# Optimization experiments

Measured on AMD Instinct MI355X. Metric: run time of the kernel, lower is better.

## Reference

```python
import jax, jax.numpy as jnp
import numpy as np

OUT_F = 8192
IN_F = 8192
RANK = 32
N_TOK = 128


def _pack_ternary(w_q):
    """Pack int8 ternary {-1,0,+1} [out,in] -> uint8 [out,in//4], LSB-first 2-bit codes."""
    enc = (w_q.astype(np.int32) + 1).astype(np.uint8).reshape(w_q.shape[0], -1, 4)
    packed = enc[:, :, 0] | (enc[:, :, 1] << 2) | (enc[:, :, 2] << 4) | (enc[:, :, 3] << 6)
    return packed


def setup_inputs() -> dict:
    key = jax.random.key(0)
    kx, kw, ks, ka, kb, kbias = jax.random.split(key, 6)
    x = jax.random.normal(kx, (N_TOK, IN_F), dtype=jnp.float32)
    # ternary weights in {-1,0,+1}
    w_q = np.asarray(jax.random.randint(kw, (OUT_F, IN_F), -1, 2, dtype=jnp.int32), dtype=np.int8)
    weight_packed = jnp.asarray(_pack_ternary(w_q), dtype=jnp.uint8)
    scale = jax.random.uniform(ks, (OUT_F,), dtype=jnp.float32, minval=0.01, maxval=0.05)
    lora_A = jax.random.normal(ka, (OUT_F, RANK), dtype=jnp.float32) * 0.02
    lora_B = jax.random.normal(kb, (RANK, IN_F), dtype=jnp.float32) * 0.02
    bias = jax.random.normal(kbias, (OUT_F,), dtype=jnp.float32) * 0.01
    return {"x": x, "weight_packed": weight_packed, "scale": scale,
            "lora_A": lora_A, "lora_B": lora_B, "bias": bias, "in_features": IN_F}


def _unpack_ternary(packed, in_features, dtype):
    # packed: uint8 [out, in//4]; LSB-first 2-bit codes, code-1 -> {-1,0,+1}
    p = packed.astype(jnp.int32)
    vals = jnp.stack([p & 3, (p >> 2) & 3, (p >> 4) & 3, (p >> 6) & 3], axis=-1)
    vals = vals.reshape(packed.shape[0], -1)[:, :in_features] - 1
    return vals.astype(dtype)


def reference(x, weight_packed, scale, lora_A, lora_B, bias, in_features):
    W = _unpack_ternary(weight_packed, in_features, x.dtype)  # [out, in]
    out = (x @ W.T) * scale[None, :]                          # [n, out]
    out = out + (x @ lora_B.T) @ lora_A.T                     # low-rank LoRA path
    out = out + bias
    return out
```

## Files before the change

kernel.cpp:

```cpp
#include <hip/hip_runtime.h>
#include <hip/hip_bf16.h>
#include <stdint.h>

typedef float f32x4 __attribute__((ext_vector_type(4)));
typedef __bf16 bf16x8 __attribute__((ext_vector_type(8)));
typedef unsigned short ushort8 __attribute__((ext_vector_type(8)));

#define N_TOK 128
#define OUT_F 8192
#define IN_F  8192
#define RANK  32

#define KSPLIT 16
#define KB    (IN_F / KSPLIT)
#define BK    64
#define NSTEP (KB / BK)
#define WSTRIDE 16
#define LKC   4

#define XB_OFF 0
#define TB_OFF ((size_t)N_TOK * IN_F * 2)
#define PO_OFF (TB_OFF + (size_t)LKC * N_TOK * RANK * 4)

__device__ __forceinline__ unsigned short bf16r(float f) {
    uint32_t u = __float_as_uint(f);
    return (unsigned short)((u + 0x7FFFu + ((u >> 16) & 1u)) >> 16);
}

__global__ __launch_bounds__(256) void cvt_x(const float* __restrict__ x,
                                             unsigned short* __restrict__ xb) {
    size_t i = ((size_t)blockIdx.x * 256 + threadIdx.x) * 8;
    float4 a = *(const float4*)(x + i);
    float4 b = *(const float4*)(x + i + 4);
    ushort8 o;
    o[0] = bf16r(a.x); o[1] = bf16r(a.y); o[2] = bf16r(a.z); o[3] = bf16r(a.w);
    o[4] = bf16r(b.x); o[5] = bf16r(b.y); o[6] = bf16r(b.z); o[7] = bf16r(b.w);
    *(ushort8*)(xb + i) = o;
}

__global__ __launch_bounds__(256) void lora_t(const float* __restrict__ x,
                                              const float* __restrict__ lb,
                                              float* __restrict__ tB) {
    __shared__ float ts[256][33];
    __shared__ float ps[8][32];
    const int m = blockIdx.x >> 2, kc = blockIdx.x & 3;
    const int tid = threadIdx.x;
    const int c0 = kc * 2048 + tid * 8;
    float4 xv0 = *(const float4*)(x + (size_t)m * IN_F + c0);
    float4 xv1 = *(const float4*)(x + (size_t)m * IN_F + c0 + 4);
#pragma unroll
    for (int r = 0; r < RANK; ++r) {
        const float4* bp = (const float4*)(lb + (size_t)r * IN_F + c0);
        float4 b0 = bp[0], b1 = bp[1];
        float s = xv0.x * b0.x + xv0.y * b0.y + xv0.z * b0.z + xv0.w * b0.w +
                  xv1.x * b1.x + xv1.y * b1.y + xv1.z * b1.z + xv1.w * b1.w;
        ts[tid][r] = s;
    }
    __syncthreads();
    {
        int g = tid >> 5, r = tid & 31;
        float s = 0.f;
        for (int j = 0; j < 32; ++j) s += ts[g * 32 + j][r];
        ps[g][r] = s;
    }
    __syncthreads();
    if (tid < 32) {
        float s = 0.f;
#pragma unroll
        for (int g = 0; g < 8; ++g) s += ps[g][tid];
        tB[(kc * N_TOK + m) * RANK + tid] = s;
    }
}

__device__ __forceinline__ void decodeW(int4 v, uint32_t d[8]) {
    uint32_t p = (uint32_t)v.x | ((uint32_t)v.y << 8) |
                 ((uint32_t)v.z << 16) | ((uint32_t)v.w << 24);
    const uint32_t HI = 0x403F00BFu;
    const uint32_t LO = 0x00800080u;
#pragma unroll
    for (int j = 0; j < 8; ++j) {
        uint32_t c0 = (p >> (4 * j)) & 3u;
        uint32_t c1 = (p >> (4 * j + 2)) & 3u;
        uint32_t t = c0 | (c1 << 16);
        uint32_t sel = (t | (t << 8)) + 0x04000400u;
        d[j] = __builtin_amdgcn_perm(HI, LO, sel);
    }
}

__device__ __forceinline__ int swz(int row, int col) { return col ^ ((row & 7) << 3); }

__global__ __launch_bounds__(256) void ternary_gemm(const unsigned short* __restrict__ xb,
                                                    const int* __restrict__ wp,
                                                    unsigned short* __restrict__ pO) {
    __shared__ unsigned short xs[128][64];
    __shared__ unsigned short ww[128][64];
    const int tid = threadIdx.x;
    const int nb = blockIdx.x >> 4;
    const int ks = blockIdx.x & 15;
    const int n0 = nb * 128;
    const int k0 = ks * KB;
    const int lane = tid & 63;
    const int wid = tid >> 6;
    const int wr = wid >> 1, wc = wid & 1;

    const int srow = tid >> 2;
    const int xcol = (tid & 3) * 16;
    const unsigned short* xg0 = xb + (size_t)srow * IN_F + k0 + xcol;
    const unsigned short* xg1 = xg0 + (size_t)64 * IN_F;
    const int pcol = (tid & 3) * 4;
    const int* pg0 = wp + (size_t)(n0 + srow) * (IN_F / 4) + (k0 >> 2) + pcol;
    const int* pg1 = pg0 + (size_t)64 * (IN_F / 4);

    f32x4 acc[4][4];
#pragma unroll
    for (int i = 0; i < 4; ++i)
#pragma unroll
        for (int j = 0; j < 4; ++j) acc[i][j] = (f32x4){0.f, 0.f, 0.f, 0.f};

    const int arow = lane & 15;
    const int kgrp = (lane >> 4) * 8;
    const int wc0 = swz(srow, xcol), wc1 = swz(srow, xcol + 8);

    uint4 xw0a = *(const uint4*)(xg0);
    uint4 xw0b = *(const uint4*)(xg0 + 8);
    uint4 xw1a = *(const uint4*)(xg1);
    uint4 xw1b = *(const uint4*)(xg1 + 8);
    uint32_t d0[8], d1[8];
    int4 w0A, w1A, w0B, w1B;
    {
        int4 t0 = *(const int4*)(pg0);
        int4 t1 = *(const int4*)(pg1);
        w0A = *(const int4*)(pg0 + WSTRIDE);
        w1A = *(const int4*)(pg1 + WSTRIDE);
        decodeW(t0, d0);
        decodeW(t1, d1);
    }

#pragma unroll
    for (int s = 0; s < NSTEP; ++s) {
        __syncthreads();
        *(uint4*)&xs[srow][wc0] = xw0a;
        *(uint4*)&xs[srow][wc1] = xw0b;
        *(uint4*)&xs[srow + 64][wc0] = xw1a;
        *(uint4*)&xs[srow + 64][wc1] = xw1b;
        *(uint4*)&ww[srow][wc0] = make_uint4(d0[0], d0[1], d0[2], d0[3]);
        *(uint4*)&ww[srow][wc1] = make_uint4(d0[4], d0[5], d0[6], d0[7]);
        *(uint4*)&ww[srow + 64][wc0] = make_uint4(d1[0], d1[1], d1[2], d1[3]);
        *(uint4*)&ww[srow + 64][wc1] = make_uint4(d1[4], d1[5], d1[6], d1[7]);
        if (s + 1 < NSTEP) {
            const unsigned short* a0 = xg0 + (s + 1) * BK;
            const unsigned short* a1 = xg1 + (s + 1) * BK;
            xw0a = *(const uint4*)(a0);
            xw0b = *(const uint4*)(a0 + 8);
            xw1a = *(const uint4*)(a1);
            xw1b = *(const uint4*)(a1 + 8);
        }
        if ((s & 1) == 0) {
            if (s + 2 < NSTEP) {
                w0B = *(const int4*)(pg0 + (s + 2) * WSTRIDE);
                w1B = *(const int4*)(pg1 + (s + 2) * WSTRIDE);
            }
        } else {
            if (s + 2 < NSTEP) {
                w0A = *(const int4*)(pg0 + (s + 2) * WSTRIDE);
                w1A = *(const int4*)(pg1 + (s + 2) * WSTRIDE);
            }
        }
        __syncthreads();
        if (s + 1 < NSTEP) {
            if ((s & 1) == 0) { decodeW(w0A, d0); decodeW(w1A, d1); }
            else              { decodeW(w0B, d0); decodeW(w1B, d1); }
        }
#pragma unroll
        for (int kk = 0; kk < 2; ++kk) {
            const int kcol = kk * 32 + kgrp;
            bf16x8 af[4], bfr[4];
#pragma unroll
            for (int ar = 0; ar < 4; ++ar) {
                int row = wr * 64 + ar * 16 + arow;
                af[ar] = *(const bf16x8*)&xs[row][swz(row, kcol)];
            }
#pragma unroll
            for (int br = 0; br < 4; ++br) {
                int row = wc * 64 + br * 16 + arow;
                bfr[br] = *(const bf16x8*)&ww[row][swz(row, kcol)];
            }
#pragma unroll
            for (int ar = 0; ar < 4; ++ar)
#pragma unroll
                for (int br = 0; br < 4; ++br)
                    acc[ar][br] = __builtin_amdgcn_mfma_f32_16x16x32_bf16(
                        af[ar], bfr[br], acc[ar][br], 0, 0, 0);
        }
    }

    unsigned short* po = pO + ((size_t)ks << 20);
    const int mrow = (lane >> 4) * 4;
#pragma unroll
    for (int ar = 0; ar < 4; ++ar) {
#pragma unroll
        for (int br = 0; br < 4; ++br) {
            int m = wr * 64 + ar * 16 + mrow;
            int n = n0 + wc * 64 + br * 16 + arow;
            unsigned short* pp = po + (size_t)m * OUT_F + n;
#pragma unroll
            for (int j = 0; j < 4; ++j) pp[(size_t)j * OUT_F] = bf16r(acc[ar][br][j]);
        }
    }
}

__global__ __launch_bounds__(256) void reduce_out(const unsigned short* __restrict__ pO,
                                                  const float* __restrict__ tB,
                                                  const float* __restrict__ scale,
                                                  const float* __restrict__ lora_A,
                                                  const float* __restrict__ bias,
                                                  float* __restrict__ out) {
    __shared__ float ts[4][RANK];
    int nb = blockIdx.x & 15, mg = blockIdx.x >> 4;
    int tid = threadIdx.x;
    int m0 = mg * 4;
    if (tid < 128) {
        int i = tid >> 5, r = tid & 31;
        float s = 0.f;
#pragma unroll
        for (int c = 0; c < LKC; ++c) s += tB[(c * N_TOK + m0 + i) * RANK + r];
        ts[i][r] = s;
    }
    __syncthreads();
    int n = nb * 512 + tid * 2;
    float sc0 = scale[n], sc1 = scale[n + 1];
    float bs0 = bias[n], bs1 = bias[n + 1];
    float4 a0[8], a1[8];
    const float4* ap0 = (const float4*)(lora_A + (size_t)n * RANK);
    const float4* ap1 = (const float4*)(lora_A + (size_t)(n + 1) * RANK);
#pragma unroll
    for (int q = 0; q < 8; ++q) { a0[q] = ap0[q]; a1[q] = ap1[q]; }
#pragma unroll
    for (int i = 0; i < 4; ++i) {
        int m = m0 + i;
        const unsigned short* pp = pO + (size_t)m * OUT_F + n;
        float s0 = 0.f, s1 = 0.f;
#pragma unroll
        for (int c = 0; c < KSPLIT; ++c) {
            uint32_t u = *(const uint32_t*)(pp + ((size_t)c << 20));
            s0 += __uint_as_float(u << 16);
            s1 += __uint_as_float(u & 0xFFFF0000u);
        }
        float l0 = 0.f, l1 = 0.f;
#pragma unroll
        for (int q = 0; q < 8; ++q) {
            float4 tv = *(const float4*)&ts[i][q * 4];
            l0 = fmaf(tv.x, a0[q].x, l0); l0 = fmaf(tv.y, a0[q].y, l0);
            l0 = fmaf(tv.z, a0[q].z, l0); l0 = fmaf(tv.w, a0[q].w, l0);
            l1 = fmaf(tv.x, a1[q].x, l1); l1 = fmaf(tv.y, a1[q].y, l1);
            l1 = fmaf(tv.z, a1[q].z, l1); l1 = fmaf(tv.w, a1[q].w, l1);
        }
        out[(size_t)m * OUT_F + n]     = fmaf(s0, sc0, l0 + bs0);
        out[(size_t)m * OUT_F + n + 1] = fmaf(s1, sc1, l1 + bs1);
    }
}

extern "C" void kernel_launch(void* const* d_in, const int* in_sizes, int n_in,
                              void* d_out, int out_size, void* d_ws, size_t ws_size,
                              hipStream_t stream) {
    const float* x      = (const float*)d_in[0];
    const int*   wp     = (const int*)d_in[1];
    const float* scale  = (const float*)d_in[2];
    const float* lora_A = (const float*)d_in[3];
    const float* lora_B = (const float*)d_in[4];
    const float* bias   = (const float*)d_in[5];
    float* out = (float*)d_out;

    char* ws = (char*)d_ws;
    unsigned short* xb = (unsigned short*)(ws + XB_OFF);
    float* tB = (float*)(ws + TB_OFF);
    unsigned short* pO = (unsigned short*)(ws + PO_OFF);

    cvt_x<<<(N_TOK * IN_F) / (256 * 8), 256, 0, stream>>>(x, xb);
    lora_t<<<N_TOK * LKC, 256, 0, stream>>>(x, lora_B, tB);
    ternary_gemm<<<(OUT_F / 128) * KSPLIT, 256, 0, stream>>>(xb, wp, pO);
    reduce_out<<<16 * 32, 256, 0, stream>>>(pO, tB, scale, lora_A, bias, out);
}
```

Baseline: 55.06 us.

## Double-buffer GEMM LDS tiles with direct global-to-LDS loads of pre-swizzled x

The x conversion kernel now writes activations in a tile-major, pre-swizzled bf16 layout. The GEMM can then stream each 128x64 x tile straight into LDS with global_load_lds instead of staging it through registers. LDS tiles for x and decoded weights are double-buffered, so the next step's loads and weight decode overlap the current step's MFMAs, with one barrier per step instead of two. The K split is halved to 8, which gives fewer blocks and partial outputs to reduce but longer per-block loops; the doubled LDS use may lower occupancy.

```diff
diff --git a/kernel.cpp b/kernel.cpp
--- a/kernel.cpp
+++ b/kernel.cpp
@@ -5,13 +5,16 @@
 typedef float f32x4 __attribute__((ext_vector_type(4)));
 typedef __bf16 bf16x8 __attribute__((ext_vector_type(8)));
 typedef unsigned short ushort8 __attribute__((ext_vector_type(8)));
+
+typedef const __attribute__((address_space(1))) uint32_t gu32;
+typedef __attribute__((address_space(3))) uint32_t lu32;
 
 #define N_TOK 128
 #define OUT_F 8192
 #define IN_F  8192
 #define RANK  32
 
-#define KSPLIT 16
+#define KSPLIT 8
 #define KB    (IN_F / KSPLIT)
 #define BK    64
 #define NSTEP (KB / BK)
@@ -27,15 +30,21 @@
     return (unsigned short)((u + 0x7FFFu + ((u >> 16) & 1u)) >> 16);
 }
 
+__device__ __forceinline__ int swz(int row, int col) { return col ^ ((row & 7) << 3); }
+
 __global__ __launch_bounds__(256) void cvt_x(const float* __restrict__ x,
-                                             unsigned short* __restrict__ xb) {
-    size_t i = ((size_t)blockIdx.x * 256 + threadIdx.x) * 8;
-    float4 a = *(const float4*)(x + i);
-    float4 b = *(const float4*)(x + i + 4);
+                                             unsigned short* __restrict__ xt) {
+    size_t f = (size_t)blockIdx.x * 256 + threadIdx.x;
+    int c8 = (int)(f & 7);
+    int r = (int)((f >> 3) & 127);
+    int sblk = (int)(f >> 10);
+    int k = sblk * 64 + ((c8 ^ (r & 7)) << 3);
+    const float4* sp = (const float4*)(x + (size_t)r * IN_F + k);
+    float4 a = sp[0], b = sp[1];
     ushort8 o;
     o[0] = bf16r(a.x); o[1] = bf16r(a.y); o[2] = bf16r(a.z); o[3] = bf16r(a.w);
     o[4] = bf16r(b.x); o[5] = bf16r(b.y); o[6] = bf16r(b.z); o[7] = bf16r(b.w);
-    *(ushort8*)(xb + i) = o;
+    *(ushort8*)(xt + f * 8) = o;
 }
 
 __global__ __launch_bounds__(256) void lora_t(const float* __restrict__ x,
@@ -87,29 +96,25 @@
     }
 }
 
-__device__ __forceinline__ int swz(int row, int col) { return col ^ ((row & 7) << 3); }
-
-__global__ __launch_bounds__(256) void ternary_gemm(const unsigned short* __restrict__ xb,
+__global__ __launch_bounds__(256) void ternary_gemm(const unsigned short* __restrict__ xt,
                                                     const int* __restrict__ wp,
                                                     unsigned short* __restrict__ pO) {
-    __shared__ unsigned short xs[128][64];
-    __shared__ unsigned short ww[128][64];
+    __shared__ unsigned short xs[2][128][64];
+    __shared__ unsigned short ww[2][128][64];
     const int tid = threadIdx.x;
-    const int nb = blockIdx.x >> 4;
-    const int ks = blockIdx.x & 15;
+    const int nb = blockIdx.x >> 3;
+    const int ks = blockIdx.x & 7;
     const int n0 = nb * 128;
-    const int k0 = ks * KB;
     const int lane = tid & 63;
     const int wid = tid >> 6;
     const int wr = wid >> 1, wc = wid & 1;
 
     const int srow = tid >> 2;
     const int xcol = (tid & 3) * 16;
-    const unsigned short* xg0 = xb + (size_t)srow * IN_F + k0 + xcol;
-    const unsigned short* xg1 = xg0 + (size_t)64 * IN_F;
-    const int pcol = (tid & 3) * 4;
-    const int* pg0 = wp + (size_t)(n0 + srow) * (IN_F / 4) + (k0 >> 2) + pcol;
+    const int* pg0 = wp + (size_t)(n0 + srow) * (IN_F / 4) + ks * (KB / 4) + (tid & 3) * 4;
     const int* pg1 = pg0 + (size_t)64 * (IN_F / 4);
+
+    const unsigned short* xsrc = xt + ((size_t)(ks * NSTEP) * 128 + wid * 8) * 64 + lane * 8;
 
     f32x4 acc[4][4];
 #pragma unroll
@@ -121,55 +126,51 @@
     const int kgrp = (lane >> 4) * 8;
     const int wc0 = swz(srow, xcol), wc1 = swz(srow, xcol + 8);
 
-    uint4 xw0a = *(const uint4*)(xg0);
-    uint4 xw0b = *(const uint4*)(xg0 + 8);
-    uint4 xw1a = *(const uint4*)(xg1);
-    uint4 xw1b = *(const uint4*)(xg1 + 8);
-    uint32_t d0[8], d1[8];
-    int4 w0A, w1A, w0B, w1B;
+    int4 wA0 = *(const int4*)(pg0);
+    int4 wA1 = *(const int4*)(pg1);
+#pragma unroll
+    for (int j = 0; j < 4; ++j)
+        __builtin_amdgcn_global_load_lds(
+            (gu32*)(xsrc + j * 2048),
+            (lu32*)((char*)(&xs[0][0][0]) + wid * 1024 + j * 4096), 16, 0, 0);
+    int4 wB0 = *(const int4*)(pg0 + WSTRIDE);
+    int4 wB1 = *(const int4*)(pg1 + WSTRIDE);
     {
-        int4 t0 = *(const int4*)(pg0);
-        int4 t1 = *(const int4*)(pg1);
-        w0A = *(const int4*)(pg0 + WSTRIDE);
-        w1A = *(const int4*)(pg1 + WSTRIDE);
-        decodeW(t0, d0);
-        decodeW(t1, d1);
-    }
+        uint32_t d0[8], d1[8];
+        decodeW(wA0, d0);
+        decodeW(wA1, d1);
+        *(uint4*)&ww[0][srow][wc0]      = make_uint4(d0[0], d0[1], d0[2], d0[3]);
+        *(uint4*)&ww[0][srow][wc1]      = make_uint4(d0[4], d0[5], d0[6], d0[7]);
+        *(uint4*)&ww[0][srow + 64][wc0] = make_uint4(d1[0], d1[1], d1[2], d1[3]);
+        *(uint4*)&ww[0][srow + 64][wc1] = make_uint4(d1[4], d1[5], d1[6], d1[7]);
+    }
+    __syncthreads();
 
 #pragma unroll
     for (int s = 0; s < NSTEP; ++s) {
-        __syncthreads();
-        *(uint4*)&xs[srow][wc0] = xw0a;
-        *(uint4*)&xs[srow][wc1] = xw0b;
-        *(uint4*)&xs[srow + 64][wc0] = xw1a;
-        *(uint4*)&xs[srow + 64][wc1] = xw1b;
-        *(uint4*)&ww[srow][wc0] = make_uint4(d0[0], d0[1], d0[2], d0[3]);
-        *(uint4*)&ww[srow][wc1] = make_uint4(d0[4], d0[5], d0[6], d0[7]);
-        *(uint4*)&ww[srow + 64][wc0] = make_uint4(d1[0], d1[1], d1[2], d1[3]);
-        *(uint4*)&ww[srow + 64][wc1] = make_uint4(d1[4], d1[5], d1[6], d1[7]);
+        const int cur = s & 1, nxt = cur ^ 1;
+        if (s + 2 < NSTEP) {
+            if ((s & 1) == 0) {
+                wA0 = *(const int4*)(pg0 + (s + 2) * WSTRIDE);
+                wA1 = *(const int4*)(pg1 + (s + 2) * WSTRIDE);
+            } else {
+                wB0 = *(const int4*)(pg0 + (s + 2) * WSTRIDE);
+                wB1 = *(const int4*)(pg1 + (s + 2) * WSTRIDE);
+            }
+        }
         if (s + 1 < NSTEP) {
-            const unsigned short* a0 = xg0 + (s + 1) * BK;
-            const unsigned short* a1 = xg1 + (s + 1) * BK;
-            xw0a = *(const uint4*)(a0);
-            xw0b = *(const uint4*)(a0 + 8);
-            xw1a = *(const uint4*)(a1);
-            xw1b = *(const uint4*)(a1 + 8);
-        }
-        if ((s & 1) == 0) {
-            if (s + 2 < NSTEP) {
-                w0B = *(const int4*)(pg0 + (s + 2) * WSTRIDE);
-                w1B = *(const int4*)(pg1 + (s + 2) * WSTRIDE);
-            }
-        } else {
-            if (s + 2 < NSTEP) {
-                w0A = *(const int4*)(pg0 + (s + 2) * WSTRIDE);
-                w1A = *(const int4*)(pg1 + (s + 2) * WSTRIDE);
-            }
-        }
-        __syncthreads();
-        if (s + 1 < NSTEP) {
-            if ((s & 1) == 0) { decodeW(w0A, d0); decodeW(w1A, d1); }
-            else              { decodeW(w0B, d0); decodeW(w1B, d1); }
+#pragma unroll
+            for (int j = 0; j < 4; ++j)
+                __builtin_amdgcn_global_load_lds(
+                    (gu32*)(xsrc + (size_t)(s + 1) * (128 * 64) + j * 2048),
+                    (lu32*)((char*)(&xs[nxt][0][0]) + wid * 1024 + j * 4096), 16, 0, 0);
+            uint32_t d0[8], d1[8];
+            if ((s & 1) == 0) { decodeW(wB0, d0); decodeW(wB1, d1); }
+            else              { decodeW(wA0, d0); decodeW(wA1, d1); }
+            *(uint4*)&ww[nxt][srow][wc0]      = make_uint4(d0[0], d0[1], d0[2], d0[3]);
+            *(uint4*)&ww[nxt][srow][wc1]      = make_uint4(d0[4], d0[5], d0[6], d0[7]);
+            *(uint4*)&ww[nxt][srow + 64][wc0] = make_uint4(d1[0], d1[1], d1[2], d1[3]);
+            *(uint4*)&ww[nxt][srow + 64][wc1] = make_uint4(d1[4], d1[5], d1[6], d1[7]);
         }
 #pragma unroll
         for (int kk = 0; kk < 2; ++kk) {
@@ -178,12 +179,12 @@
 #pragma unroll
             for (int ar = 0; ar < 4; ++ar) {
                 int row = wr * 64 + ar * 16 + arow;
-                af[ar] = *(const bf16x8*)&xs[row][swz(row, kcol)];
+                af[ar] = *(const bf16x8*)&xs[cur][row][swz(row, kcol)];
             }
 #pragma unroll
             for (int br = 0; br < 4; ++br) {
                 int row = wc * 64 + br * 16 + arow;
-                bfr[br] = *(const bf16x8*)&ww[row][swz(row, kcol)];
+                bfr[br] = *(const bf16x8*)&ww[cur][row][swz(row, kcol)];
             }
 #pragma unroll
             for (int ar = 0; ar < 4; ++ar)
@@ -192,6 +193,7 @@
                     acc[ar][br] = __builtin_amdgcn_mfma_f32_16x16x32_bf16(
                         af[ar], bfr[br], acc[ar][br], 0, 0, 0);
         }
+        __syncthreads();
     }
 
     unsigned short* po = pO + ((size_t)ks << 20);
@@ -272,12 +274,12 @@
     float* out = (float*)d_out;
 
     char* ws = (char*)d_ws;
-    unsigned short* xb = (unsigned short*)(ws + XB_OFF);
+    unsigned short* xt = (unsigned short*)(ws + XB_OFF);
     float* tB = (float*)(ws + TB_OFF);
     unsigned short* pO = (unsigned short*)(ws + PO_OFF);
 
-    cvt_x<<<(N_TOK * IN_F) / (256 * 8), 256, 0, stream>>>(x, xb);
+    cvt_x<<<512, 256, 0, stream>>>(x, xt);
     lora_t<<<N_TOK * LKC, 256, 0, stream>>>(x, lora_B, tB);
-    ternary_gemm<<<(OUT_F / 128) * KSPLIT, 256, 0, stream>>>(xb, wp, pO);
+    ternary_gemm<<<(OUT_F / 128) * KSPLIT, 256, 0, stream>>>(xt, wp, pO);
     reduce_out<<<16 * 32, 256, 0, stream>>>(pO, tB, scale, lora_A, bias, out);
 }
```

New measurement: 54.42 us. Within noise of the previous version (-1.2%).
